# Kernel optimization log

Measured on AMD Instinct MI355X. Metric: run time of the kernel, lower is better.

Reference implementation:

```python
import jax, jax.numpy as jnp
import numpy as np

B, L, ENC_IN, C_OUT = 8, 8192, 21, 21
D_MODEL, D_STATE, D_CONV, EXPAND = 512, 16, 4, 2
D_INNER = EXPAND * D_MODEL
DT_RANK = -(-D_MODEL // 16)  # 'auto' -> ceil(d_model/16) = 32
PRED_LEN = 720


def setup_inputs() -> dict:
    key = jax.random.key(0)
    ks = jax.random.split(key, 16)
    s = lambda k, sh, sc=0.02: jax.random.normal(k, sh, jnp.float32) * sc
    # Mamba-style dt bias init: dt ~ exp(U(log dt_min, log dt_max)), bias = softplus^{-1}(dt)
    dt = jnp.exp(jax.random.uniform(ks[9], (D_INNER,), jnp.float32,
                                    float(np.log(1e-3)), float(np.log(0.1))))
    b_dt = jnp.log(jnp.expm1(dt))
    return dict(
        x_enc=jax.random.normal(ks[0], (B, L, ENC_IN), jnp.float32),
        x_mark_enc=jax.random.normal(ks[1], (B, L, 4), jnp.float32),
        x_dec=jax.random.normal(ks[2], (B, PRED_LEN, ENC_IN), jnp.float32),
        x_mark_dec=jax.random.normal(ks[3], (B, PRED_LEN, 4), jnp.float32),
        W_embed=s(ks[4], (ENC_IN, D_MODEL)),
        b_embed=jnp.zeros((D_MODEL,), jnp.float32),
        W_in=s(ks[5], (D_MODEL, 2 * D_INNER)),
        conv_w=s(ks[6], (D_INNER, D_CONV), 0.1),
        conv_b=jnp.zeros((D_INNER,), jnp.float32),
        W_xproj=s(ks[7], (D_INNER, DT_RANK + 2 * D_STATE)),
        W_dt=s(ks[8], (DT_RANK, D_INNER), 0.1),
        b_dt=b_dt,
        A_log=jnp.log(jnp.tile(jnp.arange(1, D_STATE + 1, dtype=jnp.float32), (D_INNER, 1))),
        D=jnp.ones((D_INNER,), jnp.float32),
        W_out_ssm=s(ks[10], (D_INNER, D_MODEL)),
        W_proj=s(ks[11], (D_MODEL, C_OUT)),
        b_proj=jnp.zeros((C_OUT,), jnp.float32),
    )


def _mamba(x, W_in, conv_w, conv_b, W_xproj, W_dt, b_dt, A_log, D):
    b, l, _ = x.shape
    d_inner, d_conv = conv_w.shape
    d_state = A_log.shape[1]
    dt_rank = W_dt.shape[0]
    xz = x @ W_in                                   # [b,l,2*d_inner]
    u, z = jnp.split(xz, 2, axis=-1)
    # causal depthwise conv over time
    uc = jnp.transpose(u, (0, 2, 1))                # [b,d_inner,l]
    uc = jax.lax.conv_general_dilated(uc, conv_w[:, None, :], (1,),
                                      [(d_conv - 1, 0)],
                                      feature_group_count=d_inner)
    u = jax.nn.silu(jnp.transpose(uc, (0, 2, 1)) + conv_b)
    x_dbl = u @ W_xproj
    dt, Bm, Cm = jnp.split(x_dbl, [dt_rank, dt_rank + d_state], axis=-1)
    delta = jax.nn.softplus(dt @ W_dt + b_dt)       # [b,l,d_inner]
    A = -jnp.exp(A_log)                             # [d_inner,d_state]

    def step(h, inp):
        d_t, B_t, C_t, u_t = inp                    # [b,d_inner],[b,d_state],[b,d_state],[b,d_inner]
        dA = jnp.exp(d_t[..., None] * A)            # [b,d_inner,d_state]
        h = dA * h + (d_t * u_t)[..., None] * B_t[:, None, :]
        y = jnp.einsum('bds,bs->bd', h, C_t)
        return h, y

    h0 = jnp.zeros((b, d_inner, d_state), u.dtype)
    xs = (jnp.moveaxis(delta, 1, 0), jnp.moveaxis(Bm, 1, 0),
          jnp.moveaxis(Cm, 1, 0), jnp.moveaxis(u, 1, 0))
    _, ys = jax.lax.scan(step, h0, xs)              # ys: [l,b,d_inner]
    y = jnp.moveaxis(ys, 0, 1) + u * D
    return y * jax.nn.silu(z)


def reference(x_enc, x_mark_enc, x_dec, x_mark_dec, W_embed, b_embed, W_in,
              conv_w, conv_b, W_xproj, W_dt, b_dt, A_log, D, W_out_ssm,
              W_proj, b_proj):
    # RevIN normalize (stats detached, matching .detach() in torch)
    means = jax.lax.stop_gradient(x_enc.mean(axis=1, keepdims=True))
    xc = x_enc - means
    stdev = jax.lax.stop_gradient(jnp.sqrt(jnp.var(xc, axis=1, keepdims=True) + 1e-5))
    xn = xc / stdev
    emb = xn @ W_embed + b_embed                    # [b,L,d_model]
    y = _mamba(emb, W_in, conv_w, conv_b, W_xproj, W_dt, b_dt, A_log, D)
    y = y @ W_out_ssm                               # [b,L,d_model]
    y = y[:, -PRED_LEN:, :]                         # L >= pred_len branch
    out = y @ W_proj + b_proj                       # [b,pred_len,c_out]
    out = out * stdev[:, :1, :] + means[:, :1, :]   # RevIN denorm (c_out == enc_in)
    return out
```

## Files before the change

kernel.cpp:

```cpp
#include <hip/hip_runtime.h>
#include <hip/hip_bf16.h>
#include <stdint.h>

#define B_    8
#define L_    8192
#define CIN   21
#define DM    512
#define DI    1024
#define DS    16
#define DTR   32
#define PRED  720
#define L0    (L_ - PRED)
#define CHUNK 128
#define NCHK  64
#define NTCH  6
#define TAIL0 7424
#define NSUB  24
#define TROWS 768

typedef __bf16 bf16_t;
typedef __attribute__((ext_vector_type(4))) __bf16 bf16x4;
typedef __attribute__((ext_vector_type(8))) __bf16 bf16x8;
typedef __attribute__((ext_vector_type(4))) float f32x4;
typedef __attribute__((ext_vector_type(2))) float f32x2;

__device__ __forceinline__ void gl_lds16(const void* g, void* l) {
  __builtin_amdgcn_global_load_lds(
      (const __attribute__((address_space(1))) unsigned int*)g,
      (__attribute__((address_space(3))) unsigned int*)l, 16, 0, 0);
}

__device__ __forceinline__ float b2f(bf16_t v) { return (float)v; }
__device__ __forceinline__ bf16_t f2b(float v) { return (bf16_t)v; }

__global__ void zero_kernel(float* __restrict__ out, int n) {
  int i = blockIdx.x * 256 + threadIdx.x;
  if (i < n) out[i] = 0.f;
}

__global__ __launch_bounds__(256) void stats_kernel(const float* __restrict__ x,
                                                    float* __restrict__ stats) {
  const int b = blockIdx.x / CIN, c = blockIdx.x % CIN;
  const int tid = threadIdx.x;
  float s = 0.f, s2 = 0.f;
  for (int l = tid; l < L_; l += 256) {
    float v = x[((size_t)b * L_ + l) * CIN + c];
    s += v; s2 += v * v;
  }
  __shared__ float rs[256], rs2[256];
  rs[tid] = s; rs2[tid] = s2;
  __syncthreads();
  for (int o = 128; o > 0; o >>= 1) {
    if (tid < o) { rs[tid] += rs[tid + o]; rs2[tid] += rs2[tid + o]; }
    __syncthreads();
  }
  if (tid == 0) {
    float mean = rs[0] / (float)L_;
    float var  = rs2[0] / (float)L_ - mean * mean;
    stats[(b * CIN + c) * 2]     = mean;
    stats[(b * CIN + c) * 2 + 1] = sqrtf(var + 1e-5f);
  }
}

__global__ void tconv_kernel(const float* __restrict__ in, bf16_t* __restrict__ out,
                             int R, int C) {
  int idx = blockIdx.x * 256 + threadIdx.x;
  if (idx < R * C) {
    int r = idx / C, c = idx % C;
    out[(size_t)c * R + r] = f2b(in[idx]);
  }
}
__global__ void tconvf_kernel(const float* __restrict__ in, float* __restrict__ out,
                              int R, int C) {
  int idx = blockIdx.x * 256 + threadIdx.x;
  if (idx < R * C) {
    int r = idx / C, c = idx % C;
    out[(size_t)c * R + r] = in[idx];
  }
}

__global__ __launch_bounds__(256) void wcomb_kernel(const float* __restrict__ We,
                                                    const float* __restrict__ be,
                                                    const float* __restrict__ Win,
                                                    float* __restrict__ Wcu,
                                                    float* __restrict__ Wcz) {
  int idx = blockIdx.x * 256 + threadIdx.x;
  if (idx >= 22 * 2048) return;
  int c = idx / 2048, n = idx % 2048;
  float a = 0.f;
  if (c < 21) {
    for (int k = 0; k < DM; ++k) a = fmaf(We[c * DM + k], Win[(size_t)k * 2048 + n], a);
  } else {
    for (int k = 0; k < DM; ++k) a = fmaf(be[k], Win[(size_t)k * 2048 + n], a);
  }
  if (n < DI) Wcu[c * DI + n] = a;
  else        Wcz[c * DI + (n - DI)] = a;
}

__global__ __launch_bounds__(256) void fc_kernel(const float* __restrict__ x,
                                                 const float* __restrict__ stats,
                                                 const float* __restrict__ Wcu,
                                                 const float* __restrict__ cwT,
                                                 const float* __restrict__ cb,
                                                 bf16_t* __restrict__ u_act) {
  __shared__ float xn[11][22];
  const size_t bb = blockIdx.y;
  const float* xb = x + bb * ((size_t)L_ * CIN);
  const float* st = stats + bb * (CIN * 2);
  bf16_t* ua = u_act + bb * ((size_t)L_ * DI);
  const int r0 = blockIdx.x * 8;
  const int tid = threadIdx.x;
  for (int i = tid; i < 11 * 22; i += 256) {
    int j = i / 22, c = i % 22;
    int row = r0 - 3 + j;
    float v = 0.f;
    if (row >= 0) {
      if (c < 21) v = (xb[(size_t)row * CIN + c] - st[c * 2]) / st[c * 2 + 1];
      else v = 1.f;
    }
    xn[j][c] = v;
  }
  __syncthreads();
  const int col = tid * 4;
  f32x4 acc[11] = {};
  for (int c = 0; c < 22; ++c) {
    f32x4 w = *(const f32x4*)&Wcu[c * DI + col];
#pragma unroll
    for (int j = 0; j < 11; ++j) acc[j] += xn[j][c] * w;
  }
  f32x4 w0 = *(const f32x4*)&cwT[0 * DI + col];
  f32x4 w1 = *(const f32x4*)&cwT[1 * DI + col];
  f32x4 w2 = *(const f32x4*)&cwT[2 * DI + col];
  f32x4 w3 = *(const f32x4*)&cwT[3 * DI + col];
  f32x4 cbv = *(const f32x4*)&cb[col];
#pragma unroll
  for (int i = 0; i < 8; ++i) {
    f32x4 a = cbv + w0 * acc[i] + w1 * acc[i + 1] + w2 * acc[i + 2] + w3 * acc[i + 3];
    bf16x4 o;
#pragma unroll
    for (int e = 0; e < 4; ++e) {
      float v = a[e];
      o[e] = f2b(v / (1.f + __expf(-v)));
    }
    *(bf16x4*)&ua[(size_t)(r0 + i) * DI + col] = o;
  }
}

__global__ __launch_bounds__(256) void zfc_kernel(const float* __restrict__ x,
                                                  const float* __restrict__ stats,
                                                  const float* __restrict__ Wcz,
                                                  bf16_t* __restrict__ zbuf) {
  __shared__ float xn[22];
  const int row = blockIdx.x;
  const size_t b = blockIdx.y;
  const int tid = threadIdx.x;
  if (tid < 22) {
    int l = L0 + row;
    float v = 1.f;
    if (tid < 21)
      v = (x[(b * L_ + l) * (size_t)CIN + tid] - stats[(b * CIN + tid) * 2]) /
          stats[(b * CIN + tid) * 2 + 1];
    xn[tid] = v;
  }
  __syncthreads();
  const int col = tid * 4;
  f32x4 a = {};
  for (int c = 0; c < 22; ++c) a += xn[c] * *(const f32x4*)&Wcz[c * DI + col];
  bf16x4 o;
#pragma unroll
  for (int e = 0; e < 4; ++e) o[e] = f2b(a[e]);
  *(bf16x4*)&zbuf[(b * PRED + row) * (size_t)DI + col] = o;
}

template <int BM, int BN, int WMR, int WNR, int EPI>
__global__ __launch_bounds__(256) void gemm_kernel(
    const bf16_t* __restrict__ A, const bf16_t* __restrict__ Bt,
    bf16_t* __restrict__ O1, bf16_t* __restrict__ O1b, float* __restrict__ Of,
    int M, int N, int K, size_t sA, size_t sO1, size_t sO1b, size_t sOf) {
  __shared__ bf16_t Alds[BM][32];
  __shared__ bf16_t Blds[BN][32];
  const size_t zb = blockIdx.z;
  A += zb * sA;
  if (O1)  O1  += zb * sO1;
  if (O1b) O1b += zb * sO1b;
  if (Of)  Of  += zb * sOf;
  const int tid = threadIdx.x;
  const int wave = tid >> 6, lane = tid & 63;
  const int wm = wave >> 1, wn = wave & 1;
  const int lr = lane & 15, lk = lane >> 4;
  const int tm = blockIdx.x * BM;
  const int tn = blockIdx.y * BN;

  f32x4 acc[WMR][WNR] = {};

  const int nk = K >> 5;
  for (int ks = 0; ks < nk; ++ks) {
#pragma unroll
    for (int r = wave; r < BM / 16; r += 4)
      gl_lds16(A + (size_t)(tm + r * 16 + (lane >> 2)) * K + ks * 32 + (lane & 3) * 8,
               &Alds[r * 16][0]);
#pragma unroll
    for (int r = wave; r < BN / 16; r += 4)
      gl_lds16(Bt + (size_t)(tn + r * 16 + (lane >> 2)) * K + ks * 32 + (lane & 3) * 8,
               &Blds[r * 16][0]);
    __syncthreads();
    bf16x8 af[WMR], bfr[WNR];
#pragma unroll
    for (int mi = 0; mi < WMR; ++mi)
      af[mi] = *(const bf16x8*)(&Alds[wm * (WMR * 16) + mi * 16 + lr][lk * 8]);
#pragma unroll
    for (int ni = 0; ni < WNR; ++ni)
      bfr[ni] = *(const bf16x8*)(&Blds[wn * (WNR * 16) + ni * 16 + lr][lk * 8]);
#pragma unroll
    for (int mi = 0; mi < WMR; ++mi)
#pragma unroll
      for (int ni = 0; ni < WNR; ++ni)
        acc[mi][ni] = __builtin_amdgcn_mfma_f32_16x16x32_bf16(af[mi], bfr[ni], acc[mi][ni], 0, 0, 0);
    __syncthreads();
  }

#pragma unroll
  for (int mi = 0; mi < WMR; ++mi) {
#pragma unroll
    for (int ni = 0; ni < WNR; ++ni) {
#pragma unroll
      for (int r = 0; r < 4; ++r) {
        int row = tm + wm * (WMR * 16) + mi * 16 + lk * 4 + r;
        int col = tn + wn * (WNR * 16) + ni * 16 + lr;
        float v = acc[mi][ni][r];
        if constexpr (EPI == 0) {
          O1[(size_t)row * N + col] = f2b(v);
        } else if constexpr (EPI == 2) {
          if (col < 32) O1b[(size_t)row * 32 + col] = f2b(v);
          else          Of[(size_t)row * 32 + (col - 32)] = v;
        }
      }
    }
  }
}

__global__ __launch_bounds__(256) void scanA_kernel(
    const bf16_t* __restrict__ u_act, const bf16_t* __restrict__ dtb,
    const float* __restrict__ BC, const bf16_t* __restrict__ Wdt,
    const float* __restrict__ bdt,
    float* __restrict__ q, float* __restrict__ dsum_g,
    float* __restrict__ qs, float* __restrict__ dsums,
    bf16_t* __restrict__ dtail) {
  __shared__ __align__(16) char smem[32768];
  bf16_t (*Ul)[64] = (bf16_t(*)[64])smem;
  bf16_t (*Dt)[32] = (bf16_t(*)[32])(smem + 16384);
  bf16_t (*Wl)[32] = (bf16_t(*)[32])(smem + 24576);
  bf16_t (*Dl)[64] = (bf16_t(*)[64])(smem + 16384);
  const int tid = threadIdx.x, wave = tid >> 6, lane = tid & 63;
  const int d0 = blockIdx.x * 64, chunk = blockIdx.y;
  const size_t b = blockIdx.z;
  const bf16_t* ua = u_act + b * ((size_t)L_ * DI);
  const bf16_t* dt = dtb + b * ((size_t)L_ * 32);
  const float*  bc = BC + b * ((size_t)L_ * 32);
  const int row0 = chunk * CHUNK;
#pragma unroll
  for (int i = 0; i < 4; ++i)
    gl_lds16(ua + (size_t)(row0 + i * 32 + wave * 8 + (lane >> 3)) * DI + d0 + (lane & 7) * 8,
             &Ul[i * 32 + wave * 8][0]);
#pragma unroll
  for (int i = 0; i < 2; ++i)
    gl_lds16(dt + (size_t)(row0 + i * 64 + wave * 16 + (lane >> 2)) * 32 + (lane & 3) * 8,
             &Dt[i * 64 + wave * 16][0]);
  gl_lds16(Wdt + (size_t)(d0 + wave * 16 + (lane >> 2)) * 32 + (lane & 3) * 8,
           &Wl[wave * 16][0]);
  __syncthreads();

  const int lr = lane & 15, lk = lane >> 4;
  const int m0 = wave * 32;
  bf16x8 af0 = *(const bf16x8*)&Dt[m0 + lr][lk * 8];
  bf16x8 af1 = *(const bf16x8*)&Dt[m0 + 16 + lr][lk * 8];
  f32x4 dacc[2][4];
#pragma unroll
  for (int ni = 0; ni < 4; ++ni) {
    bf16x8 bfr = *(const bf16x8*)&Wl[ni * 16 + lr][lk * 8];
    f32x4 zz = {};
    dacc[0][ni] = __builtin_amdgcn_mfma_f32_16x16x32_bf16(af0, bfr, zz, 0, 0, 0);
    dacc[1][ni] = __builtin_amdgcn_mfma_f32_16x16x32_bf16(af1, bfr, zz, 0, 0, 0);
  }
  __syncthreads();
#pragma unroll
  for (int mi = 0; mi < 2; ++mi)
#pragma unroll
    for (int ni = 0; ni < 4; ++ni)
#pragma unroll
      for (int r = 0; r < 4; ++r) {
        int orow = m0 + mi * 16 + lk * 4 + r;
        int ocol = ni * 16 + lr;
        float xx = dacc[mi][ni][r] + bdt[d0 + ocol];
        float sp = (xx > 20.f) ? xx : log1pf(__expf(xx));
        Dl[orow][ocol] = f2b(sp);
      }
  __syncthreads();

  if (chunk >= NCHK - NTCH) {
    bf16_t* dtl = dtail + b * ((size_t)TROWS * DI) + (size_t)(row0 - TAIL0) * DI;
#pragma unroll
    for (int j = 0; j < 4; ++j) {
      int idx = j * 256 + tid;
      int rw = idx >> 3, cv = (idx & 7) * 8;
      *(bf16x8*)&dtl[(size_t)rw * DI + d0 + cv] = *(const bf16x8*)&Dl[rw][cv];
    }
  }

  f32x2 h01{}, h23{}, h45{}, h67{}, h89{}, hab{}, hcd{}, hef{};
  float dsub = 0.f;
  const int t0 = wave * 32;
#pragma unroll 4
  for (int t = 0; t < 32; ++t) {
    int ridx = __builtin_amdgcn_readfirstlane(row0 + t0 + t);
    const float* brow = bc + (size_t)ridx * 32;
    f32x2 B0 = *(const f32x2*)(brow + 0);
    f32x2 B1 = *(const f32x2*)(brow + 2);
    f32x2 B2 = *(const f32x2*)(brow + 4);
    f32x2 B3 = *(const f32x2*)(brow + 6);
    f32x2 B4 = *(const f32x2*)(brow + 8);
    f32x2 B5 = *(const f32x2*)(brow + 10);
    f32x2 B6 = *(const f32x2*)(brow + 12);
    f32x2 B7 = *(const f32x2*)(brow + 14);
    float dlt = b2f(Dl[t0 + t][lane]);
    float ut  = b2f(Ul[t0 + t][lane]);
    float rr = __expf(-dlt);
    float du = dlt * ut;
    dsub += dlt;
    float r2s = rr * rr;
    f32x2 p01 = {rr, r2s};
    f32x2 rq  = {r2s, r2s};
    f32x2 p23 = p01 * rq, p45 = p23 * rq, p67 = p45 * rq, p89 = p67 * rq,
          pab = p89 * rq, pcd = pab * rq, pef = pcd * rq;
    f32x2 du2 = {du, du};
    h01 = p01 * h01 + du2 * B0;
    h23 = p23 * h23 + du2 * B1;
    h45 = p45 * h45 + du2 * B2;
    h67 = p67 * h67 + du2 * B3;
    h89 = p89 * h89 + du2 * B4;
    hab = pab * hab + du2 * B5;
    hcd = pcd * hcd + du2 * B6;
    hef = pef * hef + du2 * B7;
  }
  if (chunk >= NCHK - NTCH) {
    int si = (chunk - (NCHK - NTCH)) * 4 + wave;
    float* qs_b = qs + b * ((size_t)NSUB * 16 * DI) + (size_t)si * 16 * DI + d0 + lane;
    float* ds_b = dsums + b * ((size_t)NSUB * DI);
    qs_b[0*DI]=h01[0];  qs_b[1*DI]=h01[1];  qs_b[2*DI]=h23[0];  qs_b[3*DI]=h23[1];
    qs_b[4*DI]=h45[0];  qs_b[5*DI]=h45[1];  qs_b[6*DI]=h67[0];  qs_b[7*DI]=h67[1];
    qs_b[8*DI]=h89[0];  qs_b[9*DI]=h89[1];  qs_b[10*DI]=hab[0]; qs_b[11*DI]=hab[1];
    qs_b[12*DI]=hcd[0]; qs_b[13*DI]=hcd[1]; qs_b[14*DI]=hef[0]; qs_b[15*DI]=hef[1];
    ds_b[(size_t)si * DI + d0 + lane] = dsub;
  }
  __syncthreads();
  float (*Hw)[16][64] = (float(*)[16][64])smem;
  float (*Dw)[64]     = (float(*)[64])(smem + 16384);
  Hw[wave][0][lane]=h01[0];  Hw[wave][1][lane]=h01[1];
  Hw[wave][2][lane]=h23[0];  Hw[wave][3][lane]=h23[1];
  Hw[wave][4][lane]=h45[0];  Hw[wave][5][lane]=h45[1];
  Hw[wave][6][lane]=h67[0];  Hw[wave][7][lane]=h67[1];
  Hw[wave][8][lane]=h89[0];  Hw[wave][9][lane]=h89[1];
  Hw[wave][10][lane]=hab[0]; Hw[wave][11][lane]=hab[1];
  Hw[wave][12][lane]=hcd[0]; Hw[wave][13][lane]=hcd[1];
  Hw[wave][14][lane]=hef[0]; Hw[wave][15][lane]=hef[1];
  Dw[wave][lane] = dsub;
  __syncthreads();
  float* q_b = q + b * ((size_t)NCHK * 16 * DI);
  float* dg_b = dsum_g + b * ((size_t)NCHK * DI);
#pragma unroll
  for (int k = 0; k < 4; ++k) {
    const int d = tid & 63;
    const int s = (tid >> 6) + 4 * k;
    const float As = (float)(s + 1);
    float h = 0.f;
#pragma unroll
    for (int w = 0; w < 4; ++w)
      h = fmaf(__expf(-Dw[w][d] * As), h, Hw[w][s][d]);
    q_b[((size_t)chunk * 16 + s) * DI + d0 + d] = h;
  }
  if (tid < 64)
    dg_b[(size_t)chunk * DI + d0 + tid] = Dw[0][tid] + Dw[1][tid] + Dw[2][tid] + Dw[3][tid];
}

__global__ __launch_bounds__(256) void scanB_kernel(const float* __restrict__ q,
                                                    const float* __restrict__ dsum_g,
                                                    const float* __restrict__ qs,
                                                    const float* __restrict__ dsums,
                                                    float* __restrict__ h0) {
  const int idx = blockIdx.x * 256 + threadIdx.x;
  const int d = idx & (DI - 1);
  const int s = (idx >> 10) & 15;
  const size_t b = idx >> 14;
  const float As = (float)(s + 1);
  const float* q_b = q + b * ((size_t)NCHK * 16 * DI);
  const float* dg_b = dsum_g + b * ((size_t)NCHK * DI);
  const float* qs_b = qs + b * ((size_t)NSUB * 16 * DI);
  const float* ds_b = dsums + b * ((size_t)NSUB * DI);
  float* h0_b = h0 + b * ((size_t)NSUB * 16 * DI);
  float h = 0.f;
#pragma unroll 4
  for (int c = 0; c < NCHK - NTCH; ++c)
    h = fmaf(__expf(-dg_b[(size_t)c * DI + d] * As), h, q_b[((size_t)c * 16 + s) * DI + d]);
#pragma unroll 8
  for (int si = 0; si < NSUB; ++si) {
    h0_b[((size_t)si * 16 + s) * DI + d] = h;
    h = fmaf(__expf(-ds_b[(size_t)si * DI + d] * As), h, qs_b[((size_t)si * 16 + s) * DI + d]);
  }
}

__global__ __launch_bounds__(256) void scanC_kernel(
    const bf16_t* __restrict__ dl, const bf16_t* __restrict__ uu,
    const float* __restrict__ xt, const float* __restrict__ h0buf,
    const float* __restrict__ Dvec, const bf16_t* __restrict__ zb,
    bf16_t* __restrict__ yg, size_t sdl_b, size_t suu_b, size_t sxt_b) {
  const int tid = threadIdx.x;
  const int d = blockIdx.x * 256 + tid;
  const int sub = blockIdx.y + 1;
  const size_t b = blockIdx.z;
  const bf16_t* dlp = dl + b * sdl_b;
  const bf16_t* uup = uu + b * suu_b;
  const float*  xtp = xt + b * sxt_b;
  const bf16_t* zp  = zb + b * ((size_t)PRED * DI);
  bf16_t* yp = yg + b * ((size_t)PRED * DI);
  const int lr0 = sub * 32;
  const float* hp = h0buf + (b * NSUB + sub) * (size_t)(16 * DI) + d;
  f32x2 h01 = {hp[0*DI], hp[1*DI]},   h23 = {hp[2*DI], hp[3*DI]},
        h45 = {hp[4*DI], hp[5*DI]},   h67 = {hp[6*DI], hp[7*DI]},
        h89 = {hp[8*DI], hp[9*DI]},   hab = {hp[10*DI], hp[11*DI]},
        hcd = {hp[12*DI], hp[13*DI]}, hef = {hp[14*DI], hp[15*DI]};
  const float Dd = Dvec[d];
#pragma unroll 4
  for (int t = 0; t < 32; ++t) {
    const int lr = lr0 + t;
    int ridx = __builtin_amdgcn_readfirstlane(lr);
    const float* brow = xtp + (size_t)ridx * 32;
    f32x2 B0 = *(const f32x2*)(brow + 0);
    f32x2 B1 = *(const f32x2*)(brow + 2);
    f32x2 B2 = *(const f32x2*)(brow + 4);
    f32x2 B3 = *(const f32x2*)(brow + 6);
    f32x2 B4 = *(const f32x2*)(brow + 8);
    f32x2 B5 = *(const f32x2*)(brow + 10);
    f32x2 B6 = *(const f32x2*)(brow + 12);
    f32x2 B7 = *(const f32x2*)(brow + 14);
    float dlt = b2f(dlp[(size_t)lr * DI + d]);
    float ut  = b2f(uup[(size_t)lr * DI + d]);
    float rr = __expf(-dlt);
    float du = dlt * ut;
    float r2s = rr * rr;
    f32x2 p01 = {rr, r2s};
    f32x2 rq  = {r2s, r2s};
    f32x2 p23 = p01 * rq, p45 = p23 * rq, p67 = p45 * rq, p89 = p67 * rq,
          pab = p89 * rq, pcd = pab * rq, pef = pcd * rq;
    f32x2 du2 = {du, du};
    h01 = p01 * h01 + du2 * B0;
    h23 = p23 * h23 + du2 * B1;
    h45 = p45 * h45 + du2 * B2;
    h67 = p67 * h67 + du2 * B3;
    h89 = p89 * h89 + du2 * B4;
    hab = pab * hab + du2 * B5;
    hcd = pcd * hcd + du2 * B6;
    hef = pef * hef + du2 * B7;
    if (lr >= 48) {
      f32x2 C0 = *(const f32x2*)(brow + 16);
      f32x2 C1 = *(const f32x2*)(brow + 18);
      f32x2 C2 = *(const f32x2*)(brow + 20);
      f32x2 C3 = *(const f32x2*)(brow + 22);
      f32x2 C4 = *(const f32x2*)(brow + 24);
      f32x2 C5 = *(const f32x2*)(brow + 26);
      f32x2 C6 = *(const f32x2*)(brow + 28);
      f32x2 C7 = *(const f32x2*)(brow + 30);
      f32x2 ya = h01 * C0;
      ya = h23 * C1 + ya; ya = h45 * C2 + ya; ya = h67 * C3 + ya;
      ya = h89 * C4 + ya; ya = hab * C5 + ya; ya = hcd * C6 + ya;
      ya = hef * C7 + ya;
      float y = ya[0] + ya[1];
      int gl = lr - 48;
      float zv = b2f(zp[(size_t)gl * DI + d]);
      float gate = zv / (1.f + __expf(-zv));
      yp[(size_t)gl * DI + d] = f2b((y + ut * Dd) * gate);
    }
  }
}

__global__ __launch_bounds__(256) void final_kernel(const bf16_t* __restrict__ y1,
                                                    const float* __restrict__ Wp,
                                                    const float* __restrict__ bp,
                                                    const float* __restrict__ stats,
                                                    float* __restrict__ out) {
  __shared__ float ys[DM];
  __shared__ float rs[8][32];
  const int row = blockIdx.x;
  const int b = row / PRED;
  const int tid = threadIdx.x;
  ys[tid] = b2f(y1[(size_t)row * DM + tid]);
  ys[tid + 256] = b2f(y1[(size_t)row * DM + tid + 256]);
  __syncthreads();
  const int c = tid & 31, ks = tid >> 5;
  float p = 0.f;
  if (c < CIN) {
    const int k0 = ks * 64;
    for (int k = 0; k < 64; ++k) p = fmaf(ys[k0 + k], Wp[(k0 + k) * CIN + c], p);
  }
  rs[ks][c] = p;
  __syncthreads();
  if (tid < CIN) {
    float a = bp[tid];
#pragma unroll
    for (int j = 0; j < 8; ++j) a += rs[j][tid];
    float mean = stats[(b * CIN + tid) * 2], sd = stats[(b * CIN + tid) * 2 + 1];
    out[(size_t)row * CIN + tid] = fmaf(a, sd, mean);
  }
}

static inline size_t padq(size_t x) { return (x + 255) & ~(size_t)255; }
struct Ptrs {
  bf16_t *u_act, *dtb, *dtail, *zbuf, *yg, *y1;
  bf16_t *Wt_xp, *Wt_dt, *Wt_out;
  float *BC, *q, *dsum, *qs, *dsums, *h0, *cwT, *Wcu, *Wcz, *stats;
  size_t total;
};
static Ptrs layout(char* ws) {
  Ptrs P; size_t off = 0;
  auto al = [&](size_t bytes) { char* p = ws + off; off += padq(bytes); return p; };
  P.u_act = (bf16_t*)al((size_t)B_ * L_ * DI * 2);
  P.dtb   = (bf16_t*)al((size_t)B_ * L_ * 32 * 2);
  P.BC    = (float*) al((size_t)B_ * L_ * 32 * 4);
  P.q     = (float*) al((size_t)B_ * NCHK * 16 * DI * 4);
  P.dsum  = (float*) al((size_t)B_ * NCHK * DI * 4);
  P.qs    = (float*) al((size_t)B_ * NSUB * 16 * DI * 4);
  P.dsums = (float*) al((size_t)B_ * NSUB * DI * 4);
  P.h0    = (float*) al((size_t)B_ * NSUB * 16 * DI * 4);
  P.dtail = (bf16_t*)al((size_t)B_ * TROWS * DI * 2);
  P.zbuf  = (bf16_t*)al((size_t)B_ * PRED * DI * 2);
  P.yg    = (bf16_t*)al((size_t)B_ * PRED * DI * 2);
  P.y1    = (bf16_t*)al((size_t)B_ * PRED * DM * 2);
  P.Wt_xp = (bf16_t*)al((size_t)64 * 1024 * 2);
  P.Wt_dt = (bf16_t*)al((size_t)1024 * 32 * 2);
  P.Wt_out= (bf16_t*)al((size_t)512 * 1024 * 2);
  P.cwT   = (float*) al((size_t)4 * DI * 4);
  P.Wcu   = (float*) al((size_t)22 * DI * 4);
  P.Wcz   = (float*) al((size_t)22 * DI * 4);
  P.stats = (float*) al((size_t)B_ * CIN * 2 * 4);
  P.total = off;
  return P;
}

extern "C" void kernel_launch(void* const* d_in, const int* in_sizes, int n_in,
                              void* d_out, int out_size, void* d_ws, size_t ws_size,
                              hipStream_t stream) {
  const float* x_enc   = (const float*)d_in[0];
  const float* W_embed = (const float*)d_in[4];
  const float* b_embed = (const float*)d_in[5];
  const float* W_in    = (const float*)d_in[6];
  const float* conv_w  = (const float*)d_in[7];
  const float* conv_b  = (const float*)d_in[8];
  const float* W_xproj = (const float*)d_in[9];
  const float* W_dt    = (const float*)d_in[10];
  const float* b_dt    = (const float*)d_in[11];
  const float* Dvec    = (const float*)d_in[13];
  const float* W_out   = (const float*)d_in[14];
  const float* W_proj  = (const float*)d_in[15];
  const float* b_proj  = (const float*)d_in[16];
  float* out = (float*)d_out;
  char* ws = (char*)d_ws;

  Ptrs P = layout(ws);
  if (P.total > ws_size) {
    zero_kernel<<<(out_size + 255) / 256, 256, 0, stream>>>(out, out_size);
    return;
  }

  stats_kernel<<<B_ * CIN, 256, 0, stream>>>(x_enc, P.stats);
  wcomb_kernel<<<(22 * 2048 + 255) / 256, 256, 0, stream>>>(W_embed, b_embed, W_in, P.Wcu, P.Wcz);
  tconv_kernel<<<(1024 * 64 + 255) / 256, 256, 0, stream>>>(W_xproj, P.Wt_xp, 1024, 64);
  tconv_kernel<<<(32 * 1024 + 255) / 256, 256, 0, stream>>>(W_dt,    P.Wt_dt, 32, 1024);
  tconv_kernel<<<(1024 * 512 + 255) / 256, 256, 0, stream>>>(W_out,   P.Wt_out, 1024, 512);
  tconvf_kernel<<<(1024 * 4 + 255) / 256, 256, 0, stream>>>(conv_w,  P.cwT, 1024, 4);

  zfc_kernel<<<dim3(PRED, B_), 256, 0, stream>>>(x_enc, P.stats, P.Wcz, P.zbuf);
  fc_kernel<<<dim3(L_ / 8, B_), 256, 0, stream>>>(x_enc, P.stats, P.Wcu, P.cwT, conv_b, P.u_act);
  gemm_kernel<32, 64, 1, 2, 2><<<dim3(L_ / 32, 1, B_), 256, 0, stream>>>(
      P.u_act, P.Wt_xp, nullptr, P.dtb, P.BC, L_, 64, DI,
      (size_t)L_ * DI, 0, (size_t)L_ * 32, (size_t)L_ * 32);
  scanA_kernel<<<dim3(DI / 64, NCHK, B_), 256, 0, stream>>>(
      P.u_act, P.dtb, P.BC, P.Wt_dt, b_dt, P.q, P.dsum, P.qs, P.dsums, P.dtail);
  scanB_kernel<<<(B_ * DI * DS) / 256, 256, 0, stream>>>(P.q, P.dsum, P.qs, P.dsums, P.h0);
  scanC_kernel<<<dim3(DI / 256, NSUB - 1, B_), 256, 0, stream>>>(
      P.dtail, P.u_act + (size_t)TAIL0 * DI, P.BC + (size_t)TAIL0 * 32, P.h0,
      Dvec, P.zbuf, P.yg,
      (size_t)TROWS * DI, (size_t)L_ * DI, (size_t)L_ * 32);
  gemm_kernel<64, 64, 2, 2, 0><<<dim3((B_ * PRED) / 64, DM / 64, 1), 256, 0, stream>>>(
      P.yg, P.Wt_out, P.y1, nullptr, nullptr, B_ * PRED, DM, DI, 0, 0, 0, 0);
  final_kernel<<<B_ * PRED, 256, 0, stream>>>(P.y1, W_proj, b_proj, P.stats, out);
}
```

Baseline: 515.0 us.

## Tile u_act, dtail and scan state buffers into 64-channel blocks

Stores the activation, tail-delta and scan partial-state buffers in a [batch][channel-block of 64][row][64] layout instead of row-major over all 1024 channels. The scan kernels then read each chunk's 64-channel slice as one contiguous block, and the first GEMM gains a templated path for the tiled A operand. The aim is to turn strided row-by-row loads and stores into contiguous streams. In exchange, the GEMM's A loads now jump between 64-column tiles, which may hurt its access pattern.

```diff
diff --git a/kernel.cpp b/kernel.cpp
--- a/kernel.cpp
+++ b/kernel.cpp
@@ -18,6 +18,13 @@
 #define NSUB  24
 #define TROWS 768
 
+#define UIDX(b, row, dblk, dl) ((((size_t)(b) * 16 + (dblk)) * L_ + (row)) * 64 + (dl))
+#define TIDX(b, row, dblk, dl) ((((size_t)(b) * 16 + (dblk)) * TROWS + (row)) * 64 + (dl))
+#define QIDX(b, c, dblk, s, dl) \
+  ((((((size_t)(b) * NCHK + (c)) * 16 + (dblk)) * 16 + (s)) * 64) + (dl))
+#define SIDX(b, si, dblk, s, dl) \
+  ((((((size_t)(b) * NSUB + (si)) * 16 + (dblk)) * 16 + (s)) * 64) + (dl))
+
 typedef __bf16 bf16_t;
 typedef __attribute__((ext_vector_type(4))) __bf16 bf16x4;
 typedef __attribute__((ext_vector_type(8))) __bf16 bf16x8;
@@ -107,7 +114,6 @@
   const size_t bb = blockIdx.y;
   const float* xb = x + bb * ((size_t)L_ * CIN);
   const float* st = stats + bb * (CIN * 2);
-  bf16_t* ua = u_act + bb * ((size_t)L_ * DI);
   const int r0 = blockIdx.x * 8;
   const int tid = threadIdx.x;
   for (int i = tid; i < 11 * 22; i += 256) {
@@ -122,6 +128,7 @@
   }
   __syncthreads();
   const int col = tid * 4;
+  const int dblk = col >> 6, dl = col & 63;
   f32x4 acc[11] = {};
   for (int c = 0; c < 22; ++c) {
     f32x4 w = *(const f32x4*)&Wcu[c * DI + col];
@@ -142,7 +149,7 @@
       float v = a[e];
       o[e] = f2b(v / (1.f + __expf(-v)));
     }
-    *(bf16x4*)&ua[(size_t)(r0 + i) * DI + col] = o;
+    *(bf16x4*)&u_act[UIDX(bb, r0 + i, dblk, dl)] = o;
   }
 }
 
@@ -172,7 +179,7 @@
   *(bf16x4*)&zbuf[(b * PRED + row) * (size_t)DI + col] = o;
 }
 
-template <int BM, int BN, int WMR, int WNR, int EPI>
+template <int BM, int BN, int WMR, int WNR, int EPI, bool ATILED = false>
 __global__ __launch_bounds__(256) void gemm_kernel(
     const bf16_t* __restrict__ A, const bf16_t* __restrict__ Bt,
     bf16_t* __restrict__ O1, bf16_t* __restrict__ O1b, float* __restrict__ Of,
@@ -196,9 +203,15 @@
   const int nk = K >> 5;
   for (int ks = 0; ks < nk; ++ks) {
 #pragma unroll
-    for (int r = wave; r < BM / 16; r += 4)
-      gl_lds16(A + (size_t)(tm + r * 16 + (lane >> 2)) * K + ks * 32 + (lane & 3) * 8,
-               &Alds[r * 16][0]);
+    for (int r = wave; r < BM / 16; r += 4) {
+      int row = tm + r * 16 + (lane >> 2);
+      if constexpr (ATILED) {
+        int kk = ks * 32 + (lane & 3) * 8;
+        gl_lds16(A + (((size_t)(kk >> 6) * L_ + row) * 64 + (kk & 63)), &Alds[r * 16][0]);
+      } else {
+        gl_lds16(A + (size_t)row * K + ks * 32 + (lane & 3) * 8, &Alds[r * 16][0]);
+      }
+    }
 #pragma unroll
     for (int r = wave; r < BN / 16; r += 4)
       gl_lds16(Bt + (size_t)(tn + r * 16 + (lane >> 2)) * K + ks * 32 + (lane & 3) * 8,
@@ -252,16 +265,17 @@
   bf16_t (*Wl)[32] = (bf16_t(*)[32])(smem + 24576);
   bf16_t (*Dl)[64] = (bf16_t(*)[64])(smem + 16384);
   const int tid = threadIdx.x, wave = tid >> 6, lane = tid & 63;
-  const int d0 = blockIdx.x * 64, chunk = blockIdx.y;
+  const int dblk = blockIdx.x, d0 = dblk * 64, chunk = blockIdx.y;
   const size_t b = blockIdx.z;
-  const bf16_t* ua = u_act + b * ((size_t)L_ * DI);
   const bf16_t* dt = dtb + b * ((size_t)L_ * 32);
   const float*  bc = BC + b * ((size_t)L_ * 32);
   const int row0 = chunk * CHUNK;
-#pragma unroll
-  for (int i = 0; i < 4; ++i)
-    gl_lds16(ua + (size_t)(row0 + i * 32 + wave * 8 + (lane >> 3)) * DI + d0 + (lane & 7) * 8,
-             &Ul[i * 32 + wave * 8][0]);
+  const bf16_t* usrc = u_act + UIDX(b, row0, dblk, 0);
+#pragma unroll
+  for (int i = 0; i < 4; ++i) {
+    int j = wave * 4 + i;
+    gl_lds16(usrc + j * 512 + lane * 8, (bf16_t*)Ul + j * 512);
+  }
 #pragma unroll
   for (int i = 0; i < 2; ++i)
     gl_lds16(dt + (size_t)(row0 + i * 64 + wave * 16 + (lane >> 2)) * 32 + (lane & 3) * 8,
@@ -298,12 +312,11 @@
   __syncthreads();
 
   if (chunk >= NCHK - NTCH) {
-    bf16_t* dtl = dtail + b * ((size_t)TROWS * DI) + (size_t)(row0 - TAIL0) * DI;
+    bf16_t* dtl = dtail + TIDX(b, row0 - TAIL0, dblk, 0);
 #pragma unroll
     for (int j = 0; j < 4; ++j) {
       int idx = j * 256 + tid;
-      int rw = idx >> 3, cv = (idx & 7) * 8;
-      *(bf16x8*)&dtl[(size_t)rw * DI + d0 + cv] = *(const bf16x8*)&Dl[rw][cv];
+      *(bf16x8*)&dtl[idx * 8] = *(const bf16x8*)&((bf16_t*)Dl)[idx * 8];
     }
   }
 
@@ -344,13 +357,12 @@
   }
   if (chunk >= NCHK - NTCH) {
     int si = (chunk - (NCHK - NTCH)) * 4 + wave;
-    float* qs_b = qs + b * ((size_t)NSUB * 16 * DI) + (size_t)si * 16 * DI + d0 + lane;
-    float* ds_b = dsums + b * ((size_t)NSUB * DI);
-    qs_b[0*DI]=h01[0];  qs_b[1*DI]=h01[1];  qs_b[2*DI]=h23[0];  qs_b[3*DI]=h23[1];
-    qs_b[4*DI]=h45[0];  qs_b[5*DI]=h45[1];  qs_b[6*DI]=h67[0];  qs_b[7*DI]=h67[1];
-    qs_b[8*DI]=h89[0];  qs_b[9*DI]=h89[1];  qs_b[10*DI]=hab[0]; qs_b[11*DI]=hab[1];
-    qs_b[12*DI]=hcd[0]; qs_b[13*DI]=hcd[1]; qs_b[14*DI]=hef[0]; qs_b[15*DI]=hef[1];
-    ds_b[(size_t)si * DI + d0 + lane] = dsub;
+    float* qsb = qs + SIDX(b, si, dblk, 0, lane);
+    qsb[0*64]=h01[0];  qsb[1*64]=h01[1];  qsb[2*64]=h23[0];  qsb[3*64]=h23[1];
+    qsb[4*64]=h45[0];  qsb[5*64]=h45[1];  qsb[6*64]=h67[0];  qsb[7*64]=h67[1];
+    qsb[8*64]=h89[0];  qsb[9*64]=h89[1];  qsb[10*64]=hab[0]; qsb[11*64]=hab[1];
+    qsb[12*64]=hcd[0]; qsb[13*64]=hcd[1]; qsb[14*64]=hef[0]; qsb[15*64]=hef[1];
+    dsums[((size_t)b * NSUB + si) * DI + d0 + lane] = dsub;
   }
   __syncthreads();
   float (*Hw)[16][64] = (float(*)[16][64])smem;
@@ -365,8 +377,7 @@
   Hw[wave][14][lane]=hef[0]; Hw[wave][15][lane]=hef[1];
   Dw[wave][lane] = dsub;
   __syncthreads();
-  float* q_b = q + b * ((size_t)NCHK * 16 * DI);
-  float* dg_b = dsum_g + b * ((size_t)NCHK * DI);
+  float* qb = q + QIDX(b, chunk, dblk, 0, 0);
 #pragma unroll
   for (int k = 0; k < 4; ++k) {
     const int d = tid & 63;
@@ -376,10 +387,11 @@
 #pragma unroll
     for (int w = 0; w < 4; ++w)
       h = fmaf(__expf(-Dw[w][d] * As), h, Hw[w][s][d]);
-    q_b[((size_t)chunk * 16 + s) * DI + d0 + d] = h;
+    qb[s * 64 + d] = h;
   }
   if (tid < 64)
-    dg_b[(size_t)chunk * DI + d0 + tid] = Dw[0][tid] + Dw[1][tid] + Dw[2][tid] + Dw[3][tid];
+    dsum_g[((size_t)b * NCHK + chunk) * DI + d0 + tid] =
+        Dw[0][tid] + Dw[1][tid] + Dw[2][tid] + Dw[3][tid];
 }
 
 __global__ __launch_bounds__(256) void scanB_kernel(const float* __restrict__ q,
@@ -391,43 +403,43 @@
   const int d = idx & (DI - 1);
   const int s = (idx >> 10) & 15;
   const size_t b = idx >> 14;
+  const int dblk = d >> 6, dl = d & 63;
   const float As = (float)(s + 1);
-  const float* q_b = q + b * ((size_t)NCHK * 16 * DI);
-  const float* dg_b = dsum_g + b * ((size_t)NCHK * DI);
-  const float* qs_b = qs + b * ((size_t)NSUB * 16 * DI);
-  const float* ds_b = dsums + b * ((size_t)NSUB * DI);
-  float* h0_b = h0 + b * ((size_t)NSUB * 16 * DI);
   float h = 0.f;
 #pragma unroll 4
-  for (int c = 0; c < NCHK - NTCH; ++c)
-    h = fmaf(__expf(-dg_b[(size_t)c * DI + d] * As), h, q_b[((size_t)c * 16 + s) * DI + d]);
+  for (int c = 0; c < NCHK - NTCH; ++c) {
+    float ds = dsum_g[(b * NCHK + c) * (size_t)DI + d];
+    float qv = q[QIDX(b, c, dblk, s, dl)];
+    h = fmaf(__expf(-ds * As), h, qv);
+  }
 #pragma unroll 8
   for (int si = 0; si < NSUB; ++si) {
-    h0_b[((size_t)si * 16 + s) * DI + d] = h;
-    h = fmaf(__expf(-ds_b[(size_t)si * DI + d] * As), h, qs_b[((size_t)si * 16 + s) * DI + d]);
+    h0[SIDX(b, si, dblk, s, dl)] = h;
+    float ds = dsums[(b * NSUB + si) * (size_t)DI + d];
+    float qv = qs[SIDX(b, si, dblk, s, dl)];
+    h = fmaf(__expf(-ds * As), h, qv);
   }
 }
 
 __global__ __launch_bounds__(256) void scanC_kernel(
-    const bf16_t* __restrict__ dl, const bf16_t* __restrict__ uu,
-    const float* __restrict__ xt, const float* __restrict__ h0buf,
+    const bf16_t* __restrict__ dtail, const bf16_t* __restrict__ u_act,
+    const float* __restrict__ BC, const float* __restrict__ h0buf,
     const float* __restrict__ Dvec, const bf16_t* __restrict__ zb,
-    bf16_t* __restrict__ yg, size_t sdl_b, size_t suu_b, size_t sxt_b) {
+    bf16_t* __restrict__ yg) {
   const int tid = threadIdx.x;
   const int d = blockIdx.x * 256 + tid;
+  const int dblk = d >> 6, dl = d & 63;
   const int sub = blockIdx.y + 1;
   const size_t b = blockIdx.z;
-  const bf16_t* dlp = dl + b * sdl_b;
-  const bf16_t* uup = uu + b * suu_b;
-  const float*  xtp = xt + b * sxt_b;
-  const bf16_t* zp  = zb + b * ((size_t)PRED * DI);
+  const float* xtp = BC + b * ((size_t)L_ * 32) + (size_t)TAIL0 * 32;
+  const bf16_t* zp = zb + b * ((size_t)PRED * DI);
   bf16_t* yp = yg + b * ((size_t)PRED * DI);
   const int lr0 = sub * 32;
-  const float* hp = h0buf + (b * NSUB + sub) * (size_t)(16 * DI) + d;
-  f32x2 h01 = {hp[0*DI], hp[1*DI]},   h23 = {hp[2*DI], hp[3*DI]},
-        h45 = {hp[4*DI], hp[5*DI]},   h67 = {hp[6*DI], hp[7*DI]},
-        h89 = {hp[8*DI], hp[9*DI]},   hab = {hp[10*DI], hp[11*DI]},
-        hcd = {hp[12*DI], hp[13*DI]}, hef = {hp[14*DI], hp[15*DI]};
+  const float* hp = h0buf + SIDX(b, sub, dblk, 0, dl);
+  f32x2 h01 = {hp[0*64], hp[1*64]},   h23 = {hp[2*64], hp[3*64]},
+        h45 = {hp[4*64], hp[5*64]},   h67 = {hp[6*64], hp[7*64]},
+        h89 = {hp[8*64], hp[9*64]},   hab = {hp[10*64], hp[11*64]},
+        hcd = {hp[12*64], hp[13*64]}, hef = {hp[14*64], hp[15*64]};
   const float Dd = Dvec[d];
 #pragma unroll 4
   for (int t = 0; t < 32; ++t) {
@@ -442,8 +454,8 @@
     f32x2 B5 = *(const f32x2*)(brow + 10);
     f32x2 B6 = *(const f32x2*)(brow + 12);
     f32x2 B7 = *(const f32x2*)(brow + 14);
-    float dlt = b2f(dlp[(size_t)lr * DI + d]);
-    float ut  = b2f(uup[(size_t)lr * DI + d]);
+    float dlt = b2f(dtail[TIDX(b, lr, dblk, dl)]);
+    float ut  = b2f(u_act[UIDX(b, TAIL0 + lr, dblk, dl)]);
     float rr = __expf(-dlt);
     float du = dlt * ut;
     float r2s = rr * rr;
@@ -579,16 +591,14 @@
 
   zfc_kernel<<<dim3(PRED, B_), 256, 0, stream>>>(x_enc, P.stats, P.Wcz, P.zbuf);
   fc_kernel<<<dim3(L_ / 8, B_), 256, 0, stream>>>(x_enc, P.stats, P.Wcu, P.cwT, conv_b, P.u_act);
-  gemm_kernel<32, 64, 1, 2, 2><<<dim3(L_ / 32, 1, B_), 256, 0, stream>>>(
+  gemm_kernel<32, 64, 1, 2, 2, true><<<dim3(L_ / 32, 1, B_), 256, 0, stream>>>(
       P.u_act, P.Wt_xp, nullptr, P.dtb, P.BC, L_, 64, DI,
       (size_t)L_ * DI, 0, (size_t)L_ * 32, (size_t)L_ * 32);
-  scanA_kernel<<<dim3(DI / 64, NCHK, B_), 256, 0, stream>>>(
+  scanA_kernel<<<dim3(16, NCHK, B_), 256, 0, stream>>>(
       P.u_act, P.dtb, P.BC, P.Wt_dt, b_dt, P.q, P.dsum, P.qs, P.dsums, P.dtail);
   scanB_kernel<<<(B_ * DI * DS) / 256, 256, 0, stream>>>(P.q, P.dsum, P.qs, P.dsums, P.h0);
   scanC_kernel<<<dim3(DI / 256, NSUB - 1, B_), 256, 0, stream>>>(
-      P.dtail, P.u_act + (size_t)TAIL0 * DI, P.BC + (size_t)TAIL0 * 32, P.h0,
-      Dvec, P.zbuf, P.yg,
-      (size_t)TROWS * DI, (size_t)L_ * DI, (size_t)L_ * 32);
+      P.dtail, P.u_act, P.BC, P.h0, Dvec, P.zbuf, P.yg);
   gemm_kernel<64, 64, 2, 2, 0><<<dim3((B_ * PRED) / 64, DM / 64, 1), 256, 0, stream>>>(
       P.yg, P.Wt_out, P.y1, nullptr, nullptr, B_ * PRED, DM, DI, 0, 0, 0, 0);
   final_kernel<<<B_ * PRED, 256, 0, stream>>>(P.y1, W_proj, b_proj, P.stats, out);
```

Measured after the change: 521.0 us. No clear change (+1.2%).
